# Optimization experiments

Hardware: AMD Instinct MI355X
Metric: run time of the kernel (lower is better)

Reference implementation:

```python
import jax, jax.numpy as jnp
import numpy as np

B, I, N, T = 256, 1024, 1024, 100
TAU = 20.0
NUM_WEIGHT_BITS = 8  # -> numLsbBits = 8 - (8-1) = 1
VMAX = 2.0**23 - 1.0
VMIN = -(2.0**23) + 1.0


def setup_inputs() -> dict:
    key = jax.random.key(0)
    k1, k2, k3 = jax.random.split(key, 3)
    input_spikes = jax.random.randint(k1, (B, I, T), 0, 2, dtype=jnp.int32)  # binary spikes
    weight = jax.random.normal(k2, (N, I), dtype=jnp.float32)
    bias = jax.random.normal(k3, (N,), dtype=jnp.float32)
    return {"input_spikes": input_spikes, "weight": weight, "bias": bias}


def _quantize(weight, bias):
    # scale_factor = 255 / max|w|; int() truncates toward zero
    scale = 255.0 / jnp.max(jnp.abs(weight))
    qw = jnp.trunc(weight * scale)
    # (x >> 1) << 1 with arithmetic shift == floor(x/2)*2
    qw = jnp.floor(qw / 2.0) * 2.0
    qw = qw * 64.0
    qb = jnp.trunc(bias * scale) * 64.0
    vth = jnp.trunc(1.0 * scale) * 64.0  # vTh option default = 1.0
    return qw, qb, vth


def reference(input_spikes, weight, bias):
    qw, qb, vth = _quantize(weight, bias)
    decay = float(int(4096 - np.exp(-1.0 / TAU) * 4096))  # int truncation, = 199
    keep = (4096.0 - decay) / 4096.0
    spikes_t = jnp.transpose(input_spikes, (2, 0, 1)).astype(jnp.float32)  # [T,B,I]

    def step(v, s):
        wi = s @ qw.T                       # [B,N]
        v = v * keep + wi + qb              # soft LIF update
        v = jnp.clip(v, VMIN, VMAX)
        spike = (v >= vth).astype(jnp.float32)
        v = jnp.where(v > vth, v - vth, v)  # soft reset (strict >)
        return v, spike

    v0 = jnp.zeros((B, N), jnp.float32)
    _, spikes = jax.lax.scan(step, v0, spikes_t)       # [T,B,N]
    out = jnp.transpose(spikes, (1, 2, 0))             # [B,N,T]
    # delay == 1: prepend zeros, drop last two -> length T-1
    out = jnp.concatenate([jnp.zeros((B, N, 1), jnp.float32), out[..., : T - 2]], axis=-1)
    return out
```

## Files before the change

kernel.cpp:

```cpp
#include <hip/hip_runtime.h>
#include <stdint.h>

#define B_ 256
#define I_ 1024
#define N_ 1024
#define T_ 100
#define TP_ 128
#define TOUT 99
#define BN_ 64
#define KEEP (3897.0f/4096.0f)
#define VMAXF 8388607.0f
#define VMINF (-8388607.0f)

typedef __attribute__((ext_vector_type(4))) int i32x4;

#define WS_MAX 0
#define WS_QB  4096
#define WS_QW  8192
#define WS_ST  (8192 + 1024*1024 + 4096)

__global__ void maxabs_k(const float* __restrict__ w, unsigned* __restrict__ mx) {
  float m = 0.f;
  int stride = gridDim.x * blockDim.x;
  for (int i = blockIdx.x * blockDim.x + threadIdx.x; i < N_ * I_; i += stride)
    m = fmaxf(m, fabsf(w[i]));
  #pragma unroll
  for (int off = 32; off > 0; off >>= 1)
    m = fmaxf(m, __shfl_xor(m, off));
  if ((threadIdx.x & 63) == 0) atomicMax(mx, __float_as_uint(m));
}

__global__ void quant_k(const float* __restrict__ w, const float* __restrict__ bias,
                        const unsigned* __restrict__ mx,
                        signed char* __restrict__ qw, float* __restrict__ qb) {
  const float scale = 255.0f / __uint_as_float(*mx);
  int gid = blockIdx.x * blockDim.x + threadIdx.x;
  int stride = gridDim.x * blockDim.x;
  for (int idx = gid; idx < N_ * I_; idx += stride) {
    int qi = (int)truncf(__fmul_rn(w[idx], scale));
    qw[idx] = (signed char)(qi >> 1);
  }
  if (gid < N_)
    qb[gid] = truncf(__fmul_rn(bias[gid], scale)) * 64.0f;
}

__global__ void spk_transpose_k(const int* __restrict__ spk, signed char* __restrict__ st) {
  __shared__ unsigned char tile[TP_][80];
  const int b = blockIdx.y;
  const int i0 = blockIdx.x * 64;
  for (int idx = threadIdx.x; idx < 28 * 64; idx += 256)
    tile[100 + (idx >> 6)][idx & 63] = 0;
  for (int idx = threadIdx.x; idx < 64 * 25; idx += 256) {
    int il = idx / 25, c = idx - il * 25;
    const int4 v = *(const int4*)(spk + ((size_t)(b * I_ + i0 + il)) * T_ + 4 * c);
    int t = 4 * c;
    tile[t + 0][il] = (unsigned char)v.x;
    tile[t + 1][il] = (unsigned char)v.y;
    tile[t + 2][il] = (unsigned char)v.z;
    tile[t + 3][il] = (unsigned char)v.w;
  }
  __syncthreads();
  for (int idx = threadIdx.x; idx < 128 * 4; idx += 256) {
    int t = idx >> 2, q = idx & 3;
    uint4 u = *(const uint4*)&tile[t][q * 16];
    *(uint4*)(st + ((size_t)(b * 128 + t)) * I_ + i0 + q * 16) = u;
  }
}

__global__ __launch_bounds__(256, 4)
void gemm_scan_k(const signed char* __restrict__ st,
                 const signed char* __restrict__ qw,
                 const float* __restrict__ qb,
                 const unsigned* __restrict__ mx,
                 float* __restrict__ out) {
  __shared__ __align__(16) char smem[128 * 65 * 4];

  const int bid = blockIdx.x;
  const int swz = (bid & 7) * 512 + (bid >> 3);
  const int b  = swz >> 4;
  const int n0 = (swz & 15) * BN_;

  const int tid  = threadIdx.x;
  const int lane = tid & 63;
  const int wv   = tid >> 6;
  const int wr = wv >> 1, wc = wv & 1;
  const int lrow = lane & 15;
  const int ls   = lane >> 4;

  i32x4 acc[4][2];
  #pragma unroll
  for (int i = 0; i < 4; ++i)
    #pragma unroll
    for (int j = 0; j < 2; ++j)
      acc[i][j] = (i32x4){0, 0, 0, 0};

  const char* stB = (const char*)st + (size_t)b * TP_ * I_;
  const char* qwB = (const char*)qw + (size_t)n0 * I_;

  const char* gA[2]; const char* gB1;
  #pragma unroll
  for (int j = 0; j < 2; ++j) {
    int slot = j * 256 + tid;
    int row = slot >> 2, s = slot & 3;
    gA[j] = stB + (size_t)row * I_ + ((s ^ ((row >> 1) & 3)) << 4);
  }
  { int slot = tid;
    int row = slot >> 2, s = slot & 3;
    gB1 = qwB + (size_t)row * I_ + ((s ^ ((row >> 1) & 3)) << 4); }

  int offA[4], offB[2];
  #pragma unroll
  for (int mi = 0; mi < 4; ++mi) {
    int row = wr * 64 + mi * 16 + lrow;
    offA[mi] = row * 64 + ((ls ^ ((row >> 1) & 3)) << 4);
  }
  #pragma unroll
  for (int ni = 0; ni < 2; ++ni) {
    int row = wc * 32 + ni * 16 + lrow;
    offB[ni] = 8192 + row * 64 + ((ls ^ ((row >> 1) & 3)) << 4);
  }

  #define STAGE(bufbase, ksrc) do {                                                   \
    const int g_ = (ksrc) * 64;                                                       \
    __builtin_amdgcn_global_load_lds(                                                 \
        (const __attribute__((address_space(1))) void*)(gA[0] + g_),                  \
        (__attribute__((address_space(3))) void*)(smem + (bufbase) + wv * 1024), 16, 0, 0); \
    __builtin_amdgcn_global_load_lds(                                                 \
        (const __attribute__((address_space(1))) void*)(gA[1] + g_),                  \
        (__attribute__((address_space(3))) void*)(smem + (bufbase) + 4096 + wv * 1024), 16, 0, 0); \
    __builtin_amdgcn_global_load_lds(                                                 \
        (const __attribute__((address_space(1))) void*)(gB1 + g_),                    \
        (__attribute__((address_space(3))) void*)(smem + (bufbase) + 8192 + wv * 1024), 16, 0, 0); \
  } while (0)

  STAGE(0, 0);
  int p = 0;
  for (int ks = 0; ks < 16; ++ks) {
    STAGE(12288 - p, (ks + 1) & 15);
    __builtin_amdgcn_sched_barrier(0);
    asm volatile("s_waitcnt vmcnt(3)" ::: "memory");
    __builtin_amdgcn_s_barrier();
    __builtin_amdgcn_sched_barrier(0);

    i32x4 af[4], bf[2];
    #pragma unroll
    for (int mi = 0; mi < 4; ++mi) af[mi] = *(const i32x4*)(smem + p + offA[mi]);
    #pragma unroll
    for (int ni = 0; ni < 2; ++ni) bf[ni] = *(const i32x4*)(smem + p + offB[ni]);
    asm volatile("s_waitcnt lgkmcnt(0)" ::: "memory");
    __builtin_amdgcn_sched_barrier(0);
    __builtin_amdgcn_s_barrier();

    #pragma unroll
    for (int mi = 0; mi < 4; ++mi)
      #pragma unroll
      for (int ni = 0; ni < 2; ++ni)
        acc[mi][ni] = __builtin_amdgcn_mfma_i32_16x16x64_i8(af[mi], bf[ni], acc[mi][ni], 0, 0, 0);
    p = 12288 - p;
  }

  asm volatile("s_waitcnt vmcnt(0)" ::: "memory");
  __builtin_amdgcn_sched_barrier(0);
  __builtin_amdgcn_s_barrier();

  float* WI = (float*)smem;
  #pragma unroll
  for (int mi = 0; mi < 4; ++mi) {
    int row = wr * 64 + mi * 16 + (lane >> 4) * 4;
    #pragma unroll
    for (int ni = 0; ni < 2; ++ni) {
      int col = wc * 32 + ni * 16 + (lane & 15);
      #pragma unroll
      for (int j = 0; j < 4; ++j)
        WI[(row + j) * 65 + col] = 128.0f * (float)acc[mi][ni][j];
    }
  }
  __syncthreads();

  if (tid < BN_) {
    const float scale = 255.0f / __uint_as_float(*mx);
    const float vth = truncf(scale) * 64.0f;
    const float qbn = qb[n0 + tid];
    float v = 0.f;
    float* orow = out + (size_t)(b * N_ + n0 + tid) * TOUT;
    orow[0] = 0.0f;
    for (int t = 0; t < 98; ++t) {
      float wi = WI[t * 65 + tid];
      v = __fadd_rn(__fadd_rn(__fmul_rn(v, KEEP), wi), qbn);
      v = fminf(fmaxf(v, VMINF), VMAXF);
      orow[t + 1] = (v >= vth) ? 1.0f : 0.0f;
      if (v > vth) v = __fsub_rn(v, vth);
    }
  }
}

extern "C" void kernel_launch(void* const* d_in, const int* in_sizes, int n_in,
                              void* d_out, int out_size, void* d_ws, size_t ws_size,
                              hipStream_t stream) {
  const int*   spikes = (const int*)d_in[0];
  const float* weight = (const float*)d_in[1];
  const float* bias   = (const float*)d_in[2];
  float* out = (float*)d_out;
  char* ws = (char*)d_ws;

  unsigned*    mx = (unsigned*)(ws + WS_MAX);
  float*       qb = (float*)(ws + WS_QB);
  signed char* qw = (signed char*)(ws + WS_QW);
  signed char* st = (signed char*)(ws + WS_ST);

  hipMemsetAsync(mx, 0, 4, stream);
  maxabs_k<<<256, 256, 0, stream>>>(weight, mx);
  quant_k<<<1024, 256, 0, stream>>>(weight, bias, mx, qw, qb);
  spk_transpose_k<<<dim3(16, 256), 256, 0, stream>>>(spikes, st);
  gemm_scan_k<<<4096, 256, 0, stream>>>(st, qw, qb, mx, out);
}
```

Before: 298.0 us.

## Widen GEMM N-tile to 128 and fuse maxabs into spike transpose kernel

The GEMM+scan kernel now covers 128 neurons per block instead of 64, using two accumulator sets so each loaded spike tile feeds twice the MFMA work, and the grid is halved. The scan epilogue runs in two halves through the shared WI buffer. Separately, the max-abs reduction is folded into the transpose launch as an extra column of blocks, removing one kernel launch. The costs are more registers per thread, which may hurt occupancy, and a longer serial scan epilogue per block.

```diff
diff --git a/kernel.cpp b/kernel.cpp
--- a/kernel.cpp
+++ b/kernel.cpp
@@ -7,7 +7,6 @@
 #define T_ 100
 #define TP_ 128
 #define TOUT 99
-#define BN_ 64
 #define KEEP (3897.0f/4096.0f)
 #define VMAXF 8388607.0f
 #define VMINF (-8388607.0f)
@@ -18,17 +17,6 @@
 #define WS_QB  4096
 #define WS_QW  8192
 #define WS_ST  (8192 + 1024*1024 + 4096)
-
-__global__ void maxabs_k(const float* __restrict__ w, unsigned* __restrict__ mx) {
-  float m = 0.f;
-  int stride = gridDim.x * blockDim.x;
-  for (int i = blockIdx.x * blockDim.x + threadIdx.x; i < N_ * I_; i += stride)
-    m = fmaxf(m, fabsf(w[i]));
-  #pragma unroll
-  for (int off = 32; off > 0; off >>= 1)
-    m = fmaxf(m, __shfl_xor(m, off));
-  if ((threadIdx.x & 63) == 0) atomicMax(mx, __float_as_uint(m));
-}
 
 __global__ void quant_k(const float* __restrict__ w, const float* __restrict__ bias,
                         const unsigned* __restrict__ mx,
@@ -44,7 +32,18 @@
     qb[gid] = truncf(__fmul_rn(bias[gid], scale)) * 64.0f;
 }
 
-__global__ void spk_transpose_k(const int* __restrict__ spk, signed char* __restrict__ st) {
+__global__ void spk_transpose_maxabs_k(const int* __restrict__ spk, signed char* __restrict__ st,
+                                       const float* __restrict__ w, unsigned* __restrict__ mx) {
+  if (blockIdx.x == 16) {
+    float m = 0.f;
+    for (int i = blockIdx.y * 256 + threadIdx.x; i < N_ * I_; i += 256 * 256)
+      m = fmaxf(m, fabsf(w[i]));
+    #pragma unroll
+    for (int off = 32; off > 0; off >>= 1)
+      m = fmaxf(m, __shfl_xor(m, off));
+    if ((threadIdx.x & 63) == 0) atomicMax(mx, __float_as_uint(m));
+    return;
+  }
   __shared__ unsigned char tile[TP_][80];
   const int b = blockIdx.y;
   const int i0 = blockIdx.x * 64;
@@ -73,12 +72,12 @@
                  const float* __restrict__ qb,
                  const unsigned* __restrict__ mx,
                  float* __restrict__ out) {
-  __shared__ __align__(16) char smem[128 * 65 * 4];
+  __shared__ __align__(16) char smem[33280];
 
   const int bid = blockIdx.x;
-  const int swz = (bid & 7) * 512 + (bid >> 3);
-  const int b  = swz >> 4;
-  const int n0 = (swz & 15) * BN_;
+  const int swz = (bid & 7) * 256 + (bid >> 3);
+  const int b  = swz >> 3;
+  const int n0 = (swz & 7) * 128;
 
   const int tid  = threadIdx.x;
   const int lane = tid & 63;
@@ -87,26 +86,25 @@
   const int lrow = lane & 15;
   const int ls   = lane >> 4;
 
-  i32x4 acc[4][2];
+  i32x4 acc0[4][2], acc1[4][2];
   #pragma unroll
   for (int i = 0; i < 4; ++i)
     #pragma unroll
-    for (int j = 0; j < 2; ++j)
-      acc[i][j] = (i32x4){0, 0, 0, 0};
+    for (int j = 0; j < 2; ++j) { acc0[i][j] = (i32x4){0,0,0,0}; acc1[i][j] = (i32x4){0,0,0,0}; }
 
   const char* stB = (const char*)st + (size_t)b * TP_ * I_;
   const char* qwB = (const char*)qw + (size_t)n0 * I_;
 
-  const char* gA[2]; const char* gB1;
+  const char* gA[2]; const char* gB0; const char* gB1;
   #pragma unroll
   for (int j = 0; j < 2; ++j) {
     int slot = j * 256 + tid;
     int row = slot >> 2, s = slot & 3;
     gA[j] = stB + (size_t)row * I_ + ((s ^ ((row >> 1) & 3)) << 4);
   }
-  { int slot = tid;
-    int row = slot >> 2, s = slot & 3;
-    gB1 = qwB + (size_t)row * I_ + ((s ^ ((row >> 1) & 3)) << 4); }
+  { int row = tid >> 2, s = tid & 3;
+    gB0 = qwB + (size_t)row * I_ + ((s ^ ((row >> 1) & 3)) << 4);
+    gB1 = gB0 + (size_t)64 * I_; }
 
   int offA[4], offB[2];
   #pragma unroll
@@ -129,24 +127,30 @@
         (const __attribute__((address_space(1))) void*)(gA[1] + g_),                  \
         (__attribute__((address_space(3))) void*)(smem + (bufbase) + 4096 + wv * 1024), 16, 0, 0); \
     __builtin_amdgcn_global_load_lds(                                                 \
+        (const __attribute__((address_space(1))) void*)(gB0 + g_),                    \
+        (__attribute__((address_space(3))) void*)(smem + (bufbase) + 8192 + wv * 1024), 16, 0, 0); \
+    __builtin_amdgcn_global_load_lds(                                                 \
         (const __attribute__((address_space(1))) void*)(gB1 + g_),                    \
-        (__attribute__((address_space(3))) void*)(smem + (bufbase) + 8192 + wv * 1024), 16, 0, 0); \
+        (__attribute__((address_space(3))) void*)(smem + (bufbase) + 12288 + wv * 1024), 16, 0, 0); \
   } while (0)
 
   STAGE(0, 0);
   int p = 0;
   for (int ks = 0; ks < 16; ++ks) {
-    STAGE(12288 - p, (ks + 1) & 15);
+    STAGE(16384 - p, (ks + 1) & 15);
     __builtin_amdgcn_sched_barrier(0);
-    asm volatile("s_waitcnt vmcnt(3)" ::: "memory");
+    asm volatile("s_waitcnt vmcnt(4)" ::: "memory");
     __builtin_amdgcn_s_barrier();
     __builtin_amdgcn_sched_barrier(0);
 
-    i32x4 af[4], bf[2];
+    i32x4 af[4], bf0[2], bf1[2];
     #pragma unroll
     for (int mi = 0; mi < 4; ++mi) af[mi] = *(const i32x4*)(smem + p + offA[mi]);
     #pragma unroll
-    for (int ni = 0; ni < 2; ++ni) bf[ni] = *(const i32x4*)(smem + p + offB[ni]);
+    for (int ni = 0; ni < 2; ++ni) {
+      bf0[ni] = *(const i32x4*)(smem + p + offB[ni]);
+      bf1[ni] = *(const i32x4*)(smem + p + offB[ni] + 4096);
+    }
     asm volatile("s_waitcnt lgkmcnt(0)" ::: "memory");
     __builtin_amdgcn_sched_barrier(0);
     __builtin_amdgcn_s_barrier();
@@ -154,9 +158,11 @@
     #pragma unroll
     for (int mi = 0; mi < 4; ++mi)
       #pragma unroll
-      for (int ni = 0; ni < 2; ++ni)
-        acc[mi][ni] = __builtin_amdgcn_mfma_i32_16x16x64_i8(af[mi], bf[ni], acc[mi][ni], 0, 0, 0);
-    p = 12288 - p;
+      for (int ni = 0; ni < 2; ++ni) {
+        acc0[mi][ni] = __builtin_amdgcn_mfma_i32_16x16x64_i8(af[mi], bf0[ni], acc0[mi][ni], 0, 0, 0);
+        acc1[mi][ni] = __builtin_amdgcn_mfma_i32_16x16x64_i8(af[mi], bf1[ni], acc1[mi][ni], 0, 0, 0);
+      }
+    p = 16384 - p;
   }
 
   asm volatile("s_waitcnt vmcnt(0)" ::: "memory");
@@ -164,33 +170,38 @@
   __builtin_amdgcn_s_barrier();
 
   float* WI = (float*)smem;
-  #pragma unroll
-  for (int mi = 0; mi < 4; ++mi) {
-    int row = wr * 64 + mi * 16 + (lane >> 4) * 4;
-    #pragma unroll
-    for (int ni = 0; ni < 2; ++ni) {
-      int col = wc * 32 + ni * 16 + (lane & 15);
+  const float scale = 255.0f / __uint_as_float(*mx);
+  const float vth = truncf(scale) * 64.0f;
+  #pragma unroll
+  for (int half = 0; half < 2; ++half) {
+    #pragma unroll
+    for (int mi = 0; mi < 4; ++mi) {
+      int row = wr * 64 + mi * 16 + (lane >> 4) * 4;
       #pragma unroll
-      for (int j = 0; j < 4; ++j)
-        WI[(row + j) * 65 + col] = 128.0f * (float)acc[mi][ni][j];
+      for (int ni = 0; ni < 2; ++ni) {
+        int col = wc * 32 + ni * 16 + (lane & 15);
+        #pragma unroll
+        for (int j = 0; j < 4; ++j)
+          WI[(row + j) * 65 + col] =
+              128.0f * (float)(half ? acc1[mi][ni][j] : acc0[mi][ni][j]);
+      }
     }
-  }
-  __syncthreads();
-
-  if (tid < BN_) {
-    const float scale = 255.0f / __uint_as_float(*mx);
-    const float vth = truncf(scale) * 64.0f;
-    const float qbn = qb[n0 + tid];
-    float v = 0.f;
-    float* orow = out + (size_t)(b * N_ + n0 + tid) * TOUT;
-    orow[0] = 0.0f;
-    for (int t = 0; t < 98; ++t) {
-      float wi = WI[t * 65 + tid];
-      v = __fadd_rn(__fadd_rn(__fmul_rn(v, KEEP), wi), qbn);
-      v = fminf(fmaxf(v, VMINF), VMAXF);
-      orow[t + 1] = (v >= vth) ? 1.0f : 0.0f;
-      if (v > vth) v = __fsub_rn(v, vth);
+    __syncthreads();
+    if (tid < 64) {
+      const int n_idx = n0 + half * 64 + tid;
+      const float qbn = qb[n_idx];
+      float v = 0.f;
+      float* orow = out + (size_t)(b * N_ + n_idx) * TOUT;
+      orow[0] = 0.0f;
+      for (int t = 0; t < 98; ++t) {
+        float wi = WI[t * 65 + tid];
+        v = __fadd_rn(__fadd_rn(__fmul_rn(v, KEEP), wi), qbn);
+        v = fminf(fmaxf(v, VMINF), VMAXF);
+        orow[t + 1] = (v >= vth) ? 1.0f : 0.0f;
+        if (v > vth) v = __fsub_rn(v, vth);
+      }
     }
+    __syncthreads();
   }
 }
 
@@ -209,8 +220,7 @@
   signed char* st = (signed char*)(ws + WS_ST);
 
   hipMemsetAsync(mx, 0, 4, stream);
-  maxabs_k<<<256, 256, 0, stream>>>(weight, mx);
+  spk_transpose_maxabs_k<<<dim3(17, 256), 256, 0, stream>>>(spikes, st, weight, mx);
   quant_k<<<1024, 256, 0, stream>>>(weight, bias, mx, qw, qb);
-  spk_transpose_k<<<dim3(16, 256), 256, 0, stream>>>(spikes, st);
-  gemm_scan_k<<<4096, 256, 0, stream>>>(st, qw, qb, mx, out);
-}
+  gemm_scan_k<<<2048, 256, 0, stream>>>(st, qw, qb, mx, out);
+}
```

Result: faster. 273.9 us (-8.1%).
